# Optimization experiments

Hardware: AMD Instinct MI355X
Metric: run time of the kernel (lower is better)

Reference implementation:

```python
import jax, jax.numpy as jnp
import numpy as np

NUM_HEADS = 8
LN_EPS = 1e-8


def setup_inputs() -> dict:
    key = jax.random.key(0)
    ks = jax.random.split(key, 10)
    B, Sq, Sk, D, U = 8, 1024, 1024, 512, 512
    s = 1.0 / np.sqrt(D)
    return {
        "queries": jax.random.normal(ks[0], (B, Sq, D), jnp.float32),
        "keys": jax.random.normal(ks[1], (B, Sk, D), jnp.float32),
        "Wq": jax.random.normal(ks[2], (D, U), jnp.float32) * s,
        "bq": jnp.zeros((U,), jnp.float32),
        "Wk": jax.random.normal(ks[3], (D, U), jnp.float32) * s,
        "bk": jnp.zeros((U,), jnp.float32),
        "Wv": jax.random.normal(ks[4], (D, U), jnp.float32) * s,
        "bv": jnp.zeros((U,), jnp.float32),
        "gamma": jnp.ones((U,), jnp.float32),
        "beta": jnp.zeros((U,), jnp.float32),
    }


def reference(queries, keys, Wq, bq, Wk, bk, Wv, bv, gamma, beta):
    H = NUM_HEADS
    B, Sq, _ = queries.shape
    Sk = keys.shape[1]
    U = Wq.shape[1]
    Dh = U // H

    # ReLU-activated Q/K/V projections
    Q = jax.nn.relu(queries @ Wq + bq)   # [B,Sq,U]
    K = jax.nn.relu(keys @ Wk + bk)      # [B,Sk,U]
    V = jax.nn.relu(keys @ Wv + bv)      # [B,Sk,U]

    # split_heads: concat(split(x, H, -1), 0) == head-major [H,B,S,Dh]
    Qh = Q.reshape(B, Sq, H, Dh).transpose(2, 0, 1, 3)
    Kh = K.reshape(B, Sk, H, Dh).transpose(2, 0, 1, 3)
    Vh = V.reshape(B, Sk, H, Dh).transpose(2, 0, 1, 3)

    scores = jnp.einsum('hbqd,hbkd->hbqk', Qh, Kh) / jnp.sqrt(
        jnp.asarray(Dh, scores_dtype := Qh.dtype))
    attn = jax.nn.softmax(scores, axis=-1)

    # post-softmax query mask: zero rows where sum(|q|)==0 ([B,Sq,1] bcast)
    qmask = (jnp.sum(jnp.abs(queries), axis=-1, keepdims=True) > 0)
    attn = attn * qmask.astype(attn.dtype)[None]  # [1,B,Sq,1] -> [H,B,Sq,Sk]

    out = jnp.einsum('hbqk,hbkd->hbqd', attn, Vh)  # [H,B,Sq,Dh]
    # merge_heads: inverse of split_heads
    out = out.transpose(1, 2, 0, 3).reshape(B, Sq, U)

    out = out + queries  # residual

    # LayerNorm over last axis (keras default), eps=1e-8
    mu = jnp.mean(out, axis=-1, keepdims=True)
    var = jnp.mean(jnp.square(out - mu), axis=-1, keepdims=True)
    return gamma * (out - mu) * jax.lax.rsqrt(var + LN_EPS) + beta
```

## Files before the change

### kernel.cpp

```cpp
#include <hip/hip_runtime.h>
#include <stdint.h>

#define ROWS 8192
#define UDIM 512
#define SEQ  1024
#define NH   8
#define DH   64
#define SCALE 0.125f
#define LOG2E 1.44269504f
#define SC_Q (SCALE * LOG2E)

typedef unsigned short u16;
typedef __bf16 bf16_t;
typedef bf16_t bf16x8 __attribute__((ext_vector_type(8)));
typedef float f32x4 __attribute__((ext_vector_type(4)));

__device__ __forceinline__ u16 f2bf(float f) {
    union { float f; uint32_t u; } v; v.f = f;
    uint32_t r = v.u + 0x7FFFu + ((v.u >> 16) & 1u);
    return (u16)(r >> 16);
}

__device__ __forceinline__ uint32_t pk_bf16(float a, float b) {
#if __has_builtin(__builtin_amdgcn_cvt_pk_bf16_f32)
    typedef __bf16 bf16x2_t __attribute__((ext_vector_type(2)));
    bf16x2_t r = __builtin_amdgcn_cvt_pk_bf16_f32(a, b);
    union { bf16x2_t v; uint32_t u; } c; c.v = r;
    return c.u;
#else
    return (uint32_t)f2bf(a) | ((uint32_t)f2bf(b) << 16);
#endif
}

__device__ __forceinline__ void async_ld16(u16* lds, const u16* g) {
    __builtin_amdgcn_global_load_lds((const __attribute__((address_space(1))) void*)g,
                                     (__attribute__((address_space(3))) void*)lds, 16, 0, 0);
}

__global__ void convqk_kernel(const float* __restrict__ q, const float* __restrict__ k,
                              u16* __restrict__ qb, u16* __restrict__ kb) {
    int w = threadIdx.x >> 6, lane = threadIdx.x & 63;
    int row = blockIdx.x * 4 + w;
    const float* src = (blockIdx.y == 0) ? q : k;
    u16* dst = (blockIdx.y == 0) ? qb : kb;
    const float4* s4 = (const float4*)(src + (size_t)row * UDIM);
    ushort4* o4 = (ushort4*)(dst + (size_t)row * UDIM);
    for (int j = 0; j < 2; j++) {
        float4 v = s4[j * 64 + lane];
        ushort4 b;
        b.x = f2bf(v.x); b.y = f2bf(v.y); b.z = f2bf(v.z); b.w = f2bf(v.w);
        o4[j * 64 + lane] = b;
    }
}

__global__ void transposeW_kernel(const float* __restrict__ Wq, const float* __restrict__ Wk,
                                  const float* __restrict__ Wv, u16* __restrict__ Wqt,
                                  u16* __restrict__ Wkt, u16* __restrict__ Wvt) {
    const float* in = (blockIdx.z == 0) ? Wq : (blockIdx.z == 1) ? Wk : Wv;
    u16* out = (blockIdx.z == 0) ? Wqt : (blockIdx.z == 1) ? Wkt : Wvt;
    __shared__ float tile[32][33];
    int k0 = blockIdx.y * 32, n0 = blockIdx.x * 32;
    int tx = threadIdx.x & 31, ty = threadIdx.x >> 5;
    for (int r = ty; r < 32; r += 8)
        tile[r][tx] = in[(size_t)(k0 + r) * UDIM + n0 + tx];
    __syncthreads();
    for (int r = ty; r < 32; r += 8)
        out[(size_t)(n0 + r) * UDIM + k0 + tx] = f2bf(tile[tx][r]);
}

#define CPAD 136
__global__ __launch_bounds__(256, 3) void proj_kernel(
    const u16* __restrict__ qb, const u16* __restrict__ kb,
    const u16* __restrict__ Wqt, const u16* __restrict__ Wkt, const u16* __restrict__ Wvt,
    const float* __restrict__ bq, const float* __restrict__ bk, const float* __restrict__ bv,
    u16* __restrict__ Qp, u16* __restrict__ Kp, u16* __restrict__ Vtp)
{
    const int z = blockIdx.z;
    const u16* A = (z == 0) ? qb : kb;
    const u16* W = (z == 0) ? Wqt : (z == 1) ? Wkt : Wvt;
    const float* bias = (z == 0) ? bq : (z == 1) ? bk : bv;

    __shared__ u16 smem[128 * CPAD];
    u16* a_s = smem;
    u16* b_s = smem + 4096;
    u16* c_s = smem;

    const int t = threadIdx.x;
    const int lane = t & 63, w = t >> 6;
    const int quad = lane >> 4, l15 = lane & 15;
    const int m0 = blockIdx.x * 128;
    const int n0 = blockIdx.y * 128;

    const int r0 = t >> 2;
    const int s0 = ((t & 3) ^ ((r0 >> 1) & 3)) * 8;
    const u16* Ag0 = &A[(size_t)(m0 + r0) * 512 + s0];
    const u16* Ag1 = Ag0 + (size_t)64 * 512;
    const u16* Wg0 = &W[(size_t)(n0 + r0) * 512 + s0];
    const u16* Wg1 = Wg0 + (size_t)64 * 512;
    u16* al0 = &a_s[t * 8];       u16* al1 = &a_s[(t + 256) * 8];
    u16* bl0 = &b_s[t * 8];       u16* bl1 = &b_s[(t + 256) * 8];

    int aoff[2], boff[8];
    for (int mi = 0; mi < 2; mi++) {
        int row = w * 32 + mi * 16 + l15;
        aoff[mi] = row * 32 + (quad ^ ((row >> 1) & 3)) * 8;
    }
    for (int ni = 0; ni < 8; ni++) {
        int row = ni * 16 + l15;
        boff[ni] = row * 32 + (quad ^ ((row >> 1) & 3)) * 8;
    }

    f32x4 acc[2][8];
    for (int mi = 0; mi < 2; mi++)
        for (int ni = 0; ni < 8; ni++)
            acc[mi][ni] = (f32x4){0.f, 0.f, 0.f, 0.f};

    for (int kt = 0; kt < 512; kt += 32) {
        async_ld16(al0, Ag0);  async_ld16(al1, Ag1);
        async_ld16(bl0, Wg0);  async_ld16(bl1, Wg1);
        Ag0 += 32; Ag1 += 32; Wg0 += 32; Wg1 += 32;
        __syncthreads();
        bf16x8 af[2], bf[8];
        for (int mi = 0; mi < 2; mi++) af[mi] = *(const bf16x8*)&a_s[aoff[mi]];
        for (int ni = 0; ni < 8; ni++) bf[ni] = *(const bf16x8*)&b_s[boff[ni]];
        for (int mi = 0; mi < 2; mi++)
            for (int ni = 0; ni < 8; ni++)
                acc[mi][ni] = __builtin_amdgcn_mfma_f32_16x16x32_bf16(af[mi], bf[ni], acc[mi][ni], 0, 0, 0);
        __syncthreads();
    }

    const float qscale = (z == 0) ? SC_Q : 1.f;
    float bvl[8];
    for (int ni = 0; ni < 8; ni++) bvl[ni] = bias[n0 + ni * 16 + l15];
    for (int mi = 0; mi < 2; mi++)
        for (int ni = 0; ni < 8; ni++)
            for (int r = 0; r < 4; r++)
                acc[mi][ni][r] = fmaxf(acc[mi][ni][r] + bvl[ni], 0.f) * qscale;

    if (z < 2) {
        for (int mi = 0; mi < 2; mi++)
            for (int ni = 0; ni < 8; ni++)
                for (int r = 0; r < 4; r++)
                    c_s[(w * 32 + mi * 16 + quad * 4 + r) * CPAD + ni * 16 + l15] =
                        f2bf(acc[mi][ni][r]);
        __syncthreads();
        u16* outp = (z == 0) ? Qp : Kp;
        for (int j = 0; j < 8; j++) {
            int c = t + j * 256;
            int mrow = c >> 4, col8 = c & 15;
            uint4 d = *(const uint4*)&c_s[mrow * CPAD + col8 * 8];
            *(uint4*)&outp[(size_t)(m0 + mrow) * 512 + n0 + col8 * 8] = d;
        }
    } else {
        for (int mi = 0; mi < 2; mi++)
            for (int ni = 0; ni < 8; ni++) {
                uint2 pk;
                pk.x = pk_bf16(acc[mi][ni][0], acc[mi][ni][1]);
                pk.y = pk_bf16(acc[mi][ni][2], acc[mi][ni][3]);
                *(uint2*)&c_s[(ni * 16 + l15) * CPAD + w * 32 + mi * 16 + quad * 4] = pk;
            }
        __syncthreads();
        const int bb = m0 >> 10, sk0 = m0 & 1023;
        for (int j = 0; j < 8; j++) {
            int c = t + j * 256;
            int nrow = c >> 4, col8 = c & 15;
            uint4 d = *(const uint4*)&c_s[nrow * CPAD + col8 * 8];
            *(uint4*)&Vtp[(size_t)(bb * 512 + n0 + nrow) * 1024 + sk0 + col8 * 8] = d;
        }
    }
}

__global__ __launch_bounds__(256, 3) void attn_kernel(
    const u16* __restrict__ Qb, const u16* __restrict__ Kb, const u16* __restrict__ Vt,
    float* __restrict__ O)
{
    __shared__ u16 q_s[128 * 64];
    __shared__ u16 k_s[64 * 64];
    __shared__ u16 v_s[64 * 64];
    __shared__ u16 p_s[128 * 64];

    const int t = threadIdx.x, lane = t & 63, w = t >> 6;
    const int quad = lane >> 4, l15 = lane & 15;
    const int fid = blockIdx.x;
    const int xcd = fid & 7, j = fid >> 3;
    const int hb = xcd * 8 + (j & 7);
    const int qt = j >> 3;
    const int h = hb & 7, b = hb >> 3;
    const int q0 = qt * 128;

    const int r0 = t >> 3;
    const int s0 = ((t & 7) ^ (r0 & 7)) * 8;
    u16* kl0 = &k_s[t * 8];       u16* kl1 = &k_s[(t + 256) * 8];
    u16* vl0 = &v_s[t * 8];       u16* vl1 = &v_s[(t + 256) * 8];
    const u16* kg0 = &Kb[(size_t)(b * 1024 + r0) * 512 + h * 64 + s0];
    const u16* kg1 = kg0 + (size_t)32 * 512;
    const u16* vg0 = &Vt[(size_t)(b * 512 + h * 64 + r0) * 1024 + s0];
    const u16* vg1 = vg0 + (size_t)32 * 1024;

    for (int rnd = 0; rnd < 4; rnd++) {
        int c = t + rnd * 256;
        int row = c >> 3;
        int jg = (c & 7) ^ (row & 7);
        async_ld16(&q_s[c * 8], &Qb[(size_t)(b * 1024 + q0 + row) * 512 + h * 64 + jg * 8]);
    }
    __syncthreads();

    const int prow0 = w * 16 + l15;
    bf16x8 bqf[2][2];
    for (int s = 0; s < 2; s++) {
        int row = s * 64 + prow0;
        for (int kk = 0; kk < 2; kk++)
            bqf[s][kk] = *(const bf16x8*)&q_s[row * 64 + ((kk * 4 + quad) ^ (row & 7)) * 8];
    }

    int koff[4][2], pwoff[2][4], proff[2][2];
    for (int mi = 0; mi < 4; mi++) {
        int row = mi * 16 + l15;
        koff[mi][0] = row * 64 + (quad ^ (row & 7)) * 8;
        koff[mi][1] = row * 64 + ((4 + quad) ^ (row & 7)) * 8;
    }
    for (int s = 0; s < 2; s++) {
        int row = s * 64 + prow0;
        for (int mi = 0; mi < 4; mi++)
            pwoff[s][mi] = row * 64 + ((mi * 2 + (quad >> 1)) ^ (row & 7)) * 8 + (quad & 1) * 4;
        for (int kk = 0; kk < 2; kk++)
            proff[s][kk] = row * 64 + ((kk * 4 + quad) ^ (row & 7)) * 8;
    }

    float l_lane[2] = {0.f, 0.f};
    f32x4 o_acc[2][4];
    for (int s = 0; s < 2; s++)
        for (int mi = 0; mi < 4; mi++) o_acc[s][mi] = (f32x4){0.f, 0.f, 0.f, 0.f};

    for (int it = 0; it < 16; it++) {
        async_ld16(kl0, kg0);  async_ld16(kl1, kg1);
        async_ld16(vl0, vg0);  async_ld16(vl1, vg1);
        kg0 += (size_t)64 * 512; kg1 += (size_t)64 * 512;
        vg0 += 64; vg1 += 64;
        __syncthreads();

        bf16x8 ak[4][2];
        for (int mi = 0; mi < 4; mi++) {
            ak[mi][0] = *(const bf16x8*)&k_s[koff[mi][0]];
            ak[mi][1] = *(const bf16x8*)&k_s[koff[mi][1]];
        }
        bf16x8 av[2][4];
        for (int kk = 0; kk < 2; kk++)
            for (int mi = 0; mi < 4; mi++)
                av[kk][mi] = *(const bf16x8*)&v_s[koff[mi][kk]];

        for (int s = 0; s < 2; s++) {
            f32x4 st[4];
            for (int mi = 0; mi < 4; mi++) {
                f32x4 a = (f32x4){0.f, 0.f, 0.f, 0.f};
                a = __builtin_amdgcn_mfma_f32_16x16x32_bf16(ak[mi][0], bqf[s][0], a, 0, 0, 0);
                a = __builtin_amdgcn_mfma_f32_16x16x32_bf16(ak[mi][1], bqf[s][1], a, 0, 0, 0);
                st[mi] = a;
            }
            for (int mi = 0; mi < 4; mi++) {
                float p0 = exp2f(st[mi][0]);
                float p1 = exp2f(st[mi][1]);
                float p2 = exp2f(st[mi][2]);
                float p3 = exp2f(st[mi][3]);
                l_lane[s] += (p0 + p1) + (p2 + p3);
                uint2 pk;
                pk.x = pk_bf16(p0, p1);
                pk.y = pk_bf16(p2, p3);
                *(uint2*)&p_s[pwoff[s][mi]] = pk;
            }
        }
        __syncthreads();

        for (int s = 0; s < 2; s++)
            for (int kk = 0; kk < 2; kk++) {
                bf16x8 bp = *(const bf16x8*)&p_s[proff[s][kk]];
                for (int mi = 0; mi < 4; mi++)
                    o_acc[s][mi] = __builtin_amdgcn_mfma_f32_16x16x32_bf16(av[kk][mi], bp, o_acc[s][mi], 0, 0, 0);
            }
    }

    for (int s = 0; s < 2; s++) {
        float l = l_lane[s];
        l += __shfl_xor(l, 16, 64);
        l += __shfl_xor(l, 32, 64);
        float inv = 1.f / l;
        int gq = q0 + s * 64 + prow0;
        for (int mi = 0; mi < 4; mi++) {
            float4 o;
            o.x = o_acc[s][mi][0] * inv;
            o.y = o_acc[s][mi][1] * inv;
            o.z = o_acc[s][mi][2] * inv;
            o.w = o_acc[s][mi][3] * inv;
            *(float4*)&O[(size_t)(b * 1024 + gq) * 512 + h * 64 + mi * 16 + quad * 4] = o;
        }
    }
}

__global__ void ln_kernel(const float* __restrict__ O, const float* __restrict__ q,
                          const float* __restrict__ gamma, const float* __restrict__ beta,
                          float* __restrict__ out)
{
    int w = threadIdx.x >> 6, lane = threadIdx.x & 63;
    int row = blockIdx.x * 4 + w;
    const float4* O4 = (const float4*)(O + (size_t)row * UDIM);
    const float4* q4 = (const float4*)(q + (size_t)row * UDIM);
    float4* o4 = (float4*)(out + (size_t)row * UDIM);

    float4 qq[2], oo[2];
    float am = 0.f;
    for (int j = 0; j < 2; j++) {
        qq[j] = q4[j * 64 + lane];
        oo[j] = O4[j * 64 + lane];
        am += fabsf(qq[j].x) + fabsf(qq[j].y) + fabsf(qq[j].z) + fabsf(qq[j].w);
    }
    for (int off = 32; off; off >>= 1) am += __shfl_xor(am, off, 64);
    float mask = (am > 0.f) ? 1.f : 0.f;

    float4 x[2];
    float s = 0.f, ss = 0.f;
    for (int j = 0; j < 2; j++) {
        float4 v;
        v.x = oo[j].x * mask + qq[j].x;
        v.y = oo[j].y * mask + qq[j].y;
        v.z = oo[j].z * mask + qq[j].z;
        v.w = oo[j].w * mask + qq[j].w;
        x[j] = v;
        s += v.x + v.y + v.z + v.w;
        ss += v.x * v.x + v.y * v.y + v.z * v.z + v.w * v.w;
    }
    for (int off = 32; off; off >>= 1) {
        s += __shfl_xor(s, off, 64);
        ss += __shfl_xor(ss, off, 64);
    }
    float mu = s * (1.f / 512.f);
    float var = ss * (1.f / 512.f) - mu * mu;
    float rs = rsqrtf(var + 1e-8f);
    for (int j = 0; j < 2; j++) {
        float4 g = ((const float4*)gamma)[j * 64 + lane];
        float4 bb = ((const float4*)beta)[j * 64 + lane];
        float4 v;
        v.x = g.x * (x[j].x - mu) * rs + bb.x;
        v.y = g.y * (x[j].y - mu) * rs + bb.y;
        v.z = g.z * (x[j].z - mu) * rs + bb.z;
        v.w = g.w * (x[j].w - mu) * rs + bb.w;
        o4[j * 64 + lane] = v;
    }
}

extern "C" void kernel_launch(void* const* d_in, const int* in_sizes, int n_in,
                              void* d_out, int out_size, void* d_ws, size_t ws_size,
                              hipStream_t stream)
{
    const float* queries = (const float*)d_in[0];
    const float* keys    = (const float*)d_in[1];
    const float* Wq      = (const float*)d_in[2];
    const float* bq      = (const float*)d_in[3];
    const float* Wk      = (const float*)d_in[4];
    const float* bk      = (const float*)d_in[5];
    const float* Wv      = (const float*)d_in[6];
    const float* bv      = (const float*)d_in[7];
    const float* gamma   = (const float*)d_in[8];
    const float* beta    = (const float*)d_in[9];
    float* out = (float*)d_out;

    char* ws = (char*)d_ws;
    size_t off = 0;
    auto alloc = [&](size_t bytes) {
        void* p = ws + off;
        off += (bytes + 255) & ~(size_t)255;
        return p;
    };
    u16* qb   = (u16*)alloc((size_t)ROWS * UDIM * 2);
    u16* kb   = (u16*)alloc((size_t)ROWS * UDIM * 2);
    u16* Wqt  = (u16*)alloc((size_t)UDIM * UDIM * 2);
    u16* Wkt  = (u16*)alloc((size_t)UDIM * UDIM * 2);
    u16* Wvt  = (u16*)alloc((size_t)UDIM * UDIM * 2);
    u16* Qp   = (u16*)alloc((size_t)ROWS * UDIM * 2);
    u16* Kp   = (u16*)alloc((size_t)ROWS * UDIM * 2);
    u16* Vtp  = (u16*)alloc((size_t)ROWS * UDIM * 2);
    float* Of = (float*)alloc((size_t)ROWS * UDIM * 4);

    convqk_kernel<<<dim3(ROWS / 4, 2), 256, 0, stream>>>(queries, keys, qb, kb);
    transposeW_kernel<<<dim3(16, 16, 3), 256, 0, stream>>>(Wq, Wk, Wv, Wqt, Wkt, Wvt);
    proj_kernel<<<dim3(64, 4, 3), 256, 0, stream>>>(qb, kb, Wqt, Wkt, Wvt, bq, bk, bv, Qp, Kp, Vtp);
    attn_kernel<<<512, 256, 0, stream>>>(Qp, Kp, Vtp, Of);
    ln_kernel<<<ROWS / 4, 256, 0, stream>>>(Of, queries, gamma, beta, out);
}
```

Before: 170.1 us.

## Double-buffer LDS tiles in projection and attention kernels, load Q fragments directly

Both the projection GEMM and the attention loop now use two LDS buffers. The next K-tile (or K/V tile) is prefetched asynchronously while the current one is consumed by MFMAs, so global-load latency overlaps with compute instead of stalling on a barrier every iteration. The attention kernel also drops its Q staging buffer and reads Q fragments straight from global memory, and its launch bound is relaxed from 3 to 2 blocks per CU. The trade-off is more LDS and registers per block, and possibly lower occupancy, in exchange for the overlap.

```diff
diff --git a/kernel.cpp b/kernel.cpp
--- a/kernel.cpp
+++ b/kernel.cpp
@@ -81,8 +81,6 @@
     const float* bias = (z == 0) ? bq : (z == 1) ? bk : bv;
 
     __shared__ u16 smem[128 * CPAD];
-    u16* a_s = smem;
-    u16* b_s = smem + 4096;
     u16* c_s = smem;
 
     const int t = threadIdx.x;
@@ -97,8 +95,10 @@
     const u16* Ag1 = Ag0 + (size_t)64 * 512;
     const u16* Wg0 = &W[(size_t)(n0 + r0) * 512 + s0];
     const u16* Wg1 = Wg0 + (size_t)64 * 512;
-    u16* al0 = &a_s[t * 8];       u16* al1 = &a_s[(t + 256) * 8];
-    u16* bl0 = &b_s[t * 8];       u16* bl1 = &b_s[(t + 256) * 8];
+    u16* al0[2] = { &smem[0 + t * 8],     &smem[4096 + t * 8] };
+    u16* al1[2] = { &smem[0 + (t + 256) * 8], &smem[4096 + (t + 256) * 8] };
+    u16* bl0[2] = { &smem[8192 + t * 8],      &smem[12288 + t * 8] };
+    u16* bl1[2] = { &smem[8192 + (t + 256) * 8], &smem[12288 + (t + 256) * 8] };
 
     int aoff[2], boff[8];
     for (int mi = 0; mi < 2; mi++) {
@@ -115,14 +115,22 @@
         for (int ni = 0; ni < 8; ni++)
             acc[mi][ni] = (f32x4){0.f, 0.f, 0.f, 0.f};
 
-    for (int kt = 0; kt < 512; kt += 32) {
-        async_ld16(al0, Ag0);  async_ld16(al1, Ag1);
-        async_ld16(bl0, Wg0);  async_ld16(bl1, Wg1);
-        Ag0 += 32; Ag1 += 32; Wg0 += 32; Wg1 += 32;
-        __syncthreads();
+    async_ld16(al0[0], Ag0);  async_ld16(al1[0], Ag1);
+    async_ld16(bl0[0], Wg0);  async_ld16(bl1[0], Wg1);
+    Ag0 += 32; Ag1 += 32; Wg0 += 32; Wg1 += 32;
+    __syncthreads();
+
+    for (int kt = 0; kt < 16; kt++) {
+        const int cur = kt & 1, nxt = cur ^ 1;
+        if (kt < 15) {
+            async_ld16(al0[nxt], Ag0);  async_ld16(al1[nxt], Ag1);
+            async_ld16(bl0[nxt], Wg0);  async_ld16(bl1[nxt], Wg1);
+            Ag0 += 32; Ag1 += 32; Wg0 += 32; Wg1 += 32;
+        }
+        const int ab = cur ? 4096 : 0, bb = cur ? 12288 : 8192;
         bf16x8 af[2], bf[8];
-        for (int mi = 0; mi < 2; mi++) af[mi] = *(const bf16x8*)&a_s[aoff[mi]];
-        for (int ni = 0; ni < 8; ni++) bf[ni] = *(const bf16x8*)&b_s[boff[ni]];
+        for (int mi = 0; mi < 2; mi++) af[mi] = *(const bf16x8*)&smem[ab + aoff[mi]];
+        for (int ni = 0; ni < 8; ni++) bf[ni] = *(const bf16x8*)&smem[bb + boff[ni]];
         for (int mi = 0; mi < 2; mi++)
             for (int ni = 0; ni < 8; ni++)
                 acc[mi][ni] = __builtin_amdgcn_mfma_f32_16x16x32_bf16(af[mi], bf[ni], acc[mi][ni], 0, 0, 0);
@@ -160,23 +168,22 @@
                 *(uint2*)&c_s[(ni * 16 + l15) * CPAD + w * 32 + mi * 16 + quad * 4] = pk;
             }
         __syncthreads();
-        const int bb = m0 >> 10, sk0 = m0 & 1023;
+        const int bb2 = m0 >> 10, sk0 = m0 & 1023;
         for (int j = 0; j < 8; j++) {
             int c = t + j * 256;
             int nrow = c >> 4, col8 = c & 15;
             uint4 d = *(const uint4*)&c_s[nrow * CPAD + col8 * 8];
-            *(uint4*)&Vtp[(size_t)(bb * 512 + n0 + nrow) * 1024 + sk0 + col8 * 8] = d;
-        }
-    }
-}
-
-__global__ __launch_bounds__(256, 3) void attn_kernel(
+            *(uint4*)&Vtp[(size_t)(bb2 * 512 + n0 + nrow) * 1024 + sk0 + col8 * 8] = d;
+        }
+    }
+}
+
+__global__ __launch_bounds__(256, 2) void attn_kernel(
     const u16* __restrict__ Qb, const u16* __restrict__ Kb, const u16* __restrict__ Vt,
     float* __restrict__ O)
 {
-    __shared__ u16 q_s[128 * 64];
-    __shared__ u16 k_s[64 * 64];
-    __shared__ u16 v_s[64 * 64];
+    __shared__ u16 k_s[2][64 * 64];
+    __shared__ u16 v_s[2][64 * 64];
     __shared__ u16 p_s[128 * 64];
 
     const int t = threadIdx.x, lane = t & 63, w = t >> 6;
@@ -190,27 +197,21 @@
 
     const int r0 = t >> 3;
     const int s0 = ((t & 7) ^ (r0 & 7)) * 8;
-    u16* kl0 = &k_s[t * 8];       u16* kl1 = &k_s[(t + 256) * 8];
-    u16* vl0 = &v_s[t * 8];       u16* vl1 = &v_s[(t + 256) * 8];
     const u16* kg0 = &Kb[(size_t)(b * 1024 + r0) * 512 + h * 64 + s0];
     const u16* kg1 = kg0 + (size_t)32 * 512;
     const u16* vg0 = &Vt[(size_t)(b * 512 + h * 64 + r0) * 1024 + s0];
     const u16* vg1 = vg0 + (size_t)32 * 1024;
-
-    for (int rnd = 0; rnd < 4; rnd++) {
-        int c = t + rnd * 256;
-        int row = c >> 3;
-        int jg = (c & 7) ^ (row & 7);
-        async_ld16(&q_s[c * 8], &Qb[(size_t)(b * 1024 + q0 + row) * 512 + h * 64 + jg * 8]);
-    }
-    __syncthreads();
+    u16* kd0[2] = { &k_s[0][t * 8], &k_s[1][t * 8] };
+    u16* kd1[2] = { &k_s[0][(t + 256) * 8], &k_s[1][(t + 256) * 8] };
+    u16* vd0[2] = { &v_s[0][t * 8], &v_s[1][t * 8] };
+    u16* vd1[2] = { &v_s[0][(t + 256) * 8], &v_s[1][(t + 256) * 8] };
 
     const int prow0 = w * 16 + l15;
     bf16x8 bqf[2][2];
     for (int s = 0; s < 2; s++) {
-        int row = s * 64 + prow0;
+        int qrow = b * 1024 + q0 + s * 64 + prow0;
         for (int kk = 0; kk < 2; kk++)
-            bqf[s][kk] = *(const bf16x8*)&q_s[row * 64 + ((kk * 4 + quad) ^ (row & 7)) * 8];
+            bqf[s][kk] = *(const bf16x8*)&Qb[(size_t)qrow * 512 + h * 64 + kk * 32 + quad * 8];
     }
 
     int koff[4][2], pwoff[2][4], proff[2][2];
@@ -232,22 +233,31 @@
     for (int s = 0; s < 2; s++)
         for (int mi = 0; mi < 4; mi++) o_acc[s][mi] = (f32x4){0.f, 0.f, 0.f, 0.f};
 
+    async_ld16(kd0[0], kg0);  async_ld16(kd1[0], kg1);
+    async_ld16(vd0[0], vg0);  async_ld16(vd1[0], vg1);
+    kg0 += (size_t)64 * 512; kg1 += (size_t)64 * 512;
+    vg0 += 64; vg1 += 64;
+    __syncthreads();
+
     for (int it = 0; it < 16; it++) {
-        async_ld16(kl0, kg0);  async_ld16(kl1, kg1);
-        async_ld16(vl0, vg0);  async_ld16(vl1, vg1);
-        kg0 += (size_t)64 * 512; kg1 += (size_t)64 * 512;
-        vg0 += 64; vg1 += 64;
-        __syncthreads();
+        const int cur = it & 1, nxt = cur ^ 1;
+
+        if (it < 15) {
+            async_ld16(kd0[nxt], kg0);  async_ld16(kd1[nxt], kg1);
+            async_ld16(vd0[nxt], vg0);  async_ld16(vd1[nxt], vg1);
+            kg0 += (size_t)64 * 512; kg1 += (size_t)64 * 512;
+            vg0 += 64; vg1 += 64;
+        }
 
         bf16x8 ak[4][2];
         for (int mi = 0; mi < 4; mi++) {
-            ak[mi][0] = *(const bf16x8*)&k_s[koff[mi][0]];
-            ak[mi][1] = *(const bf16x8*)&k_s[koff[mi][1]];
+            ak[mi][0] = *(const bf16x8*)&k_s[cur][koff[mi][0]];
+            ak[mi][1] = *(const bf16x8*)&k_s[cur][koff[mi][1]];
         }
         bf16x8 av[2][4];
         for (int kk = 0; kk < 2; kk++)
             for (int mi = 0; mi < 4; mi++)
-                av[kk][mi] = *(const bf16x8*)&v_s[koff[mi][kk]];
+                av[kk][mi] = *(const bf16x8*)&v_s[cur][koff[mi][kk]];
 
         for (int s = 0; s < 2; s++) {
             f32x4 st[4];
@@ -269,6 +279,7 @@
                 *(uint2*)&p_s[pwoff[s][mi]] = pk;
             }
         }
+
         __syncthreads();
 
         for (int s = 0; s < 2; s++)
@@ -277,6 +288,9 @@
                 for (int mi = 0; mi < 4; mi++)
                     o_acc[s][mi] = __builtin_amdgcn_mfma_f32_16x16x32_bf16(av[kk][mi], bp, o_acc[s][mi], 0, 0, 0);
             }
+
+        if (it < 15)
+            __syncthreads();
     }
 
     for (int s = 0; s < 2; s++) {
```

New measurement: 162.4 us. 4.5% less time.
